# Kernel optimization log

Measured on AMD Instinct MI355X. Metric: run time of the kernel, lower is better.

Reference implementation:

```python
import jax, jax.numpy as jnp
import numpy as np

N_GROUP = 4
TOPK_GROUP = 2
TOP_K = 6
ROUTED_SCALE = 2.0

T, H, E, I = 1024, 1024, 16, 704
SHARED_I = 2 * H  # n_shared_experts * hidden_size


def setup_inputs() -> dict:
    key = jax.random.key(0)
    ks = jax.random.split(key, 10)
    s = 0.02
    return {
        "h": jax.random.normal(ks[0], (T, H), jnp.float32),
        "gate_w": jax.random.normal(ks[1], (E, H), jnp.float32) * s,
        "bias": jax.random.normal(ks[2], (E,), jnp.float32) * 0.1,
        "wg": jax.random.normal(ks[3], (E, H, I), jnp.float32) * s,
        "wu": jax.random.normal(ks[4], (E, H, I), jnp.float32) * s,
        "wd": jax.random.normal(ks[5], (E, I, H), jnp.float32) * s,
        "swg": jax.random.normal(ks[6], (H, SHARED_I), jnp.float32) * s,
        "swu": jax.random.normal(ks[7], (H, SHARED_I), jnp.float32) * s,
        "swd": jax.random.normal(ks[8], (SHARED_I, H), jnp.float32) * s,
    }


def _moe_forward(h, gate_w, bias, wg, wu, wd, swg, swu, swd):
    Tn, Hd = h.shape
    En = gate_w.shape[0]
    per_group = En // N_GROUP

    # shared expert (SwiGLU MLP)
    shared = (jax.nn.silu(h @ swg) * (h @ swu)) @ swd  # [T, H]

    # gate: noaux_tc biased grouped top-k routing (DeepSeek-V3 style)
    logits = h @ gate_w.T                      # [T, E]
    scores = jax.nn.sigmoid(logits)            # [T, E]
    scores_for_choice = scores + bias[None, :]
    grp = scores_for_choice.reshape(Tn, N_GROUP, per_group)
    group_scores = jnp.sum(jax.lax.top_k(grp, 2)[0], axis=-1)   # [T, G] top-2 sum
    _, top_groups = jax.lax.top_k(group_scores, TOPK_GROUP)     # [T, TG]
    gmask = jnp.zeros((Tn, N_GROUP), bool).at[
        jnp.arange(Tn)[:, None], top_groups].set(True)
    emask = jnp.repeat(gmask, per_group, axis=1)                # [T, E]
    masked = jnp.where(emask, scores_for_choice, -jnp.inf)
    _, topk_ids = jax.lax.top_k(masked, TOP_K)                  # [T, K]
    topk_w = jnp.take_along_axis(scores, topk_ids, axis=1)      # weights from unbiased scores
    topk_w = topk_w / jnp.sum(topk_w, axis=-1, keepdims=True)   # norm_topk_prob=True

    # sparse combine weights [T, E]
    cw = jnp.zeros((Tn, En), h.dtype).at[
        jnp.arange(Tn)[:, None], topk_ids].add(topk_w)

    # per-expert SwiGLU MLPs (dense over experts, sparse combine)
    g = jnp.einsum('th,ehi->tei', h, wg)
    u = jnp.einsum('th,ehi->tei', h, wu)
    y = jnp.einsum('tei,eih->teh', jax.nn.silu(g) * u, wd)
    routed = jnp.einsum('te,teh->th', cw, y)

    return routed * ROUTED_SCALE + shared


def reference(h, gate_w, bias, wg, wu, wd, swg, swu, swd):
    return _moe_forward(h, gate_w, bias, wg, wu, wd, swg, swu, swd)
```

## Files before the change

### kernel.cpp

```cpp
#include <hip/hip_runtime.h>
#include <hip/hip_bf16.h>
#include <math.h>

#define TT 1024
#define HH 1024
#define NEXP 16
#define NI 704
#define SI 2048
#define UPMAX 506
#define WDTILES 1408
#define DNSHARED 64
#define DNMAX (DNSHARED + 504)

typedef unsigned short us;
typedef __attribute__((ext_vector_type(8))) __bf16 bf16x8;
typedef __attribute__((ext_vector_type(8))) short s16x8;
typedef __attribute__((ext_vector_type(4))) float f32x4;
typedef __attribute__((ext_vector_type(4))) unsigned short us4;

__device__ __forceinline__ us f2bf(float f) {
  unsigned u = __builtin_bit_cast(unsigned, f);
  u += 0x7fffu + ((u >> 16) & 1u);
  return (us)(u >> 16);
}

__device__ __forceinline__ int ldsOff(int row, int kg) {
  return (row * 4 + (kg ^ ((row >> 1) & 3))) * 16;
}

__device__ __forceinline__ void gl16(const void* g, void* l) {
  __builtin_amdgcn_global_load_lds((const __attribute__((address_space(1))) void*)g,
                                   (__attribute__((address_space(3))) void*)l, 16, 0, 0);
}

__device__ __forceinline__ int chunkMap(int b, int n) {
  int q = n >> 3, r = n & 7;
  int c = b & 7, i = b >> 3;
  int base = (c < r) ? c * (q + 1) : r * (q + 1) + (c - r) * q;
  return base + i;
}

__device__ __forceinline__ void tconv_tile(const float* __restrict__ inz,
                                           us* __restrict__ outz,
                                           int C, int ldo, int r0, int c0,
                                           float (*tile)[65]) {
  int t = threadIdx.x;
  int rr = t >> 4, cc = (t & 15) * 4;
  #pragma unroll
  for (int i = 0; i < 4; ++i) {
    f32x4 v = *reinterpret_cast<const f32x4*>(inz + (size_t)(r0 + rr + i * 16) * C + c0 + cc);
    tile[rr + i*16][cc + 0] = v[0];
    tile[rr + i*16][cc + 1] = v[1];
    tile[rr + i*16][cc + 2] = v[2];
    tile[rr + i*16][cc + 3] = v[3];
  }
  __syncthreads();
  int c = t >> 2, rq = t & 3;
  us lo[8], hi[8];
  #pragma unroll
  for (int j = 0; j < 8; ++j) {
    lo[j] = f2bf(tile[rq * 8 + j][c]);
    hi[j] = f2bf(tile[32 + rq * 8 + j][c]);
  }
  us* op = outz + (size_t)(c0 + c) * ldo + r0;
  *reinterpret_cast<s16x8*>(op + rq * 8)      = *reinterpret_cast<s16x8*>(&lo[0]);
  *reinterpret_cast<s16x8*>(op + 32 + rq * 8) = *reinterpret_cast<s16x8*>(&hi[0]);
}

__device__ __forceinline__ void tconv512(const float* __restrict__ inz,
                                         us* __restrict__ outz,
                                         int i0, int h0, float (*tile)[129]) {
  int t = threadIdx.x;
  int ir = t >> 3, cg = (t & 7) * 4;
  #pragma unroll
  for (int p = 0; p < 4; ++p) {
    f32x4 v = *reinterpret_cast<const f32x4*>(inz + (size_t)(i0 + ir) * HH + h0 + cg + p * 32);
    tile[ir][cg + p*32 + 0] = v[0];
    tile[ir][cg + p*32 + 1] = v[1];
    tile[ir][cg + p*32 + 2] = v[2];
    tile[ir][cg + p*32 + 3] = v[3];
  }
  __syncthreads();
  int c = t >> 2, rq = t & 3;
  us lo[8], hi[8];
  #pragma unroll
  for (int j = 0; j < 8; ++j) {
    lo[j] = f2bf(tile[rq * 8 + j][c]);
    hi[j] = f2bf(tile[32 + rq * 8 + j][c]);
  }
  us* op = outz + (size_t)(h0 + c) * NI + i0;
  *reinterpret_cast<s16x8*>(op + rq * 8)      = *reinterpret_cast<s16x8*>(&lo[0]);
  *reinterpret_cast<s16x8*>(op + 32 + rq * 8) = *reinterpret_cast<s16x8*>(&hi[0]);
}

__global__ __launch_bounds__(256) void k_prep(
    const float* __restrict__ h, const float* __restrict__ gw,
    const float* __restrict__ bias, float* __restrict__ cw,
    us* __restrict__ hb, unsigned* __restrict__ selpk,
    const float* __restrict__ wg, const float* __restrict__ wu,
    const float* __restrict__ swg, const float* __restrict__ swu,
    us* __restrict__ wgb, us* __restrict__ wub,
    us* __restrict__ swgb, us* __restrict__ swub) {
  __shared__ float tile[64][65];
  __shared__ float lgS[NEXP];
  int b = blockIdx.x;
  int tid = threadIdx.x;
  if (b < 1024) {
    int t = b;
    const float* hr = h + (size_t)t * HH;
    {
      f32x4 v = *reinterpret_cast<const f32x4*>(hr + tid * 4);
      us4 p;
      p[0] = f2bf(v[0]); p[1] = f2bf(v[1]); p[2] = f2bf(v[2]); p[3] = f2bf(v[3]);
      *reinterpret_cast<us4*>(hb + (size_t)t * HH + tid * 4) = p;
    }
    int e = tid >> 4, sub = tid & 15;
    const f32x4* hr4 = reinterpret_cast<const f32x4*>(hr);
    const f32x4* gr4 = reinterpret_cast<const f32x4*>(gw + (size_t)e * HH);
    float acc = 0.f;
    for (int i = sub; i < 256; i += 16) {
      f32x4 a = hr4[i], g = gr4[i];
      acc += a[0]*g[0] + a[1]*g[1] + a[2]*g[2] + a[3]*g[3];
    }
    acc += __shfl_down(acc, 8, 16);
    acc += __shfl_down(acc, 4, 16);
    acc += __shfl_down(acc, 2, 16);
    acc += __shfl_down(acc, 1, 16);
    if (sub == 0) lgS[e] = acc;
    __syncthreads();
    if (tid == 0) {
      float sc[NEXP], s4[NEXP];
      for (int i = 0; i < NEXP; ++i) {
        sc[i] = 1.f / (1.f + expf(-lgS[i]));
        s4[i] = sc[i] + bias[i];
      }
      float gs[4];
      for (int g = 0; g < 4; ++g) {
        float a = s4[4*g], bb = s4[4*g+1], c = s4[4*g+2], d = s4[4*g+3];
        float mx01 = fmaxf(a, bb), mn01 = fminf(a, bb);
        float mx23 = fmaxf(c, d), mn23 = fminf(c, d);
        float top = fmaxf(mx01, mx23);
        float sec = (mx01 >= mx23) ? fmaxf(mn01, mx23) : fmaxf(mn23, mx01);
        gs[g] = top + sec;
      }
      int g1 = 0;
      for (int g = 1; g < 4; ++g) if (gs[g] > gs[g1]) g1 = g;
      int g2 = -1;
      for (int g = 0; g < 4; ++g) { if (g == g1) continue; if (g2 < 0 || gs[g] > gs[g2]) g2 = g; }
      int sel[6];
      bool used[NEXP];
      for (int i = 0; i < NEXP; ++i) used[i] = false;
      float wsum = 0.f;
      for (int it = 0; it < 6; ++it) {
        int best = -1; float bv = 0.f;
        for (int i = 0; i < NEXP; ++i) {
          int grp = i >> 2;
          if ((grp != g1 && grp != g2) || used[i]) continue;
          if (best < 0 || s4[i] > bv) { best = i; bv = s4[i]; }
        }
        used[best] = true;
        sel[it] = best;
        wsum += sc[best];
      }
      float inv = 2.0f / wsum;
      unsigned pk = 0;
      for (int it = 0; it < 6; ++it) {
        pk |= (unsigned)sel[it] << (it * 4);
        cw[(size_t)t * NEXP + sel[it]] = sc[sel[it]] * inv;
      }
      selpk[t] = pk;
    }
    return;
  }
  b -= 1024;
  if (b < 2816) {
    int z = b / 176, r = b % 176;
    tconv_tile(wg + (size_t)z * HH * NI, wgb + (size_t)z * NI * HH,
               NI, HH, (r / 11) * 64, (r % 11) * 64, tile);
    return;
  }
  b -= 2816;
  if (b < 2816) {
    int z = b / 176, r = b % 176;
    tconv_tile(wu + (size_t)z * HH * NI, wub + (size_t)z * NI * HH,
               NI, HH, (r / 11) * 64, (r % 11) * 64, tile);
    return;
  }
  b -= 2816;
  if (b < 512) {
    tconv_tile(swg, swgb, SI, HH, (b >> 5) * 64, (b & 31) * 64, tile);
    return;
  }
  b -= 512;
  {
    tconv_tile(swu, swub, SI, HH, (b >> 5) * 64, (b & 31) * 64, tile);
  }
}

__global__ void k_scan(const unsigned* __restrict__ selpk,
                       int* __restrict__ cnt, int* __restrict__ list,
                       int* __restrict__ wlUp, int* __restrict__ wlDn,
                       int* __restrict__ totals) {
  int t = threadIdx.x;
  int w = t >> 6, l = t & 63;
  unsigned pk = selpk[t];
  unsigned short flags = 0;
  #pragma unroll
  for (int j = 0; j < 6; ++j) flags |= (unsigned short)(1u << ((pk >> (j * 4)) & 15));
  __shared__ int wc[16][16];
  __shared__ int pre[16][16];
  __shared__ int tiles_s[16], upo[16], dno[16], totR[2];
  #pragma unroll
  for (int e = 0; e < 16; ++e) {
    unsigned long long bal = __ballot((flags >> e) & 1);
    if (l == 0) wc[w][e] = __popcll(bal);
  }
  __syncthreads();
  if (t < 16) {
    int s = 0;
    for (int ww = 0; ww < 16; ++ww) { pre[ww][t] = s; s += wc[ww][t]; }
    cnt[t] = s;
    tiles_s[t] = (s + 127) >> 7;
  }
  __syncthreads();
  if (t < 16) {
    int uo = 0, dn = 0;
    for (int e2 = 0; e2 < t; ++e2) { uo += 6 * tiles_s[e2]; dn += 8 * tiles_s[e2]; }
    upo[t] = uo; dno[t] = dn;
    if (t == 15) { totR[0] = uo + 6 * tiles_s[15]; totR[1] = dn + 8 * tiles_s[15]; }
  }
  __syncthreads();
  {
    int te = tiles_s[w];
    for (int i = l; i < 6 * te; i += 64) {
      int nt = i / te, mt = i - nt * te;
      wlUp[upo[w] + i] = ((w * 6 + nt) << 3) | mt;
    }
    for (int i = l; i < 8 * te; i += 64) {
      int nt = i / te, mt = i - nt * te;
      wlDn[dno[w] + i] = ((w * 8 + nt) << 3) | mt;
    }
  }
  if (w == 0) {
    for (int j = l; j < 128; j += 64)
      wlUp[totR[0] + j] = ((96 + (j >> 3)) << 3) | (j & 7);
  }
  if (t == 0) { totals[0] = totR[0] + 128; totals[1] = totR[1]; }
  unsigned long long lmask = (l == 0) ? 0ull : ((~0ull) >> (64 - l));
  #pragma unroll
  for (int e = 0; e < 16; ++e) {
    bool f = (flags >> e) & 1;
    unsigned long long bal = __ballot(f);
    if (f) {
      int rank = __popcll(bal & lmask);
      int j = 0;
      #pragma unroll
      for (int jj = 0; jj < 6; ++jj) j += (((pk >> (jj * 4)) & 15) == (unsigned)e) ? jj : 0;
      list[(e << 10) + pre[w][e] + rank] = (t << 3) | j;
    }
  }
}

__global__ void k_tconvS(const float* __restrict__ swd, us* __restrict__ swdT) {
  __shared__ float tile[64][65];
  int b = blockIdx.x;
  tconv_tile(swd, swdT, HH, SI, (b >> 4) * 64, (b & 15) * 64, tile);
}

__global__ __launch_bounds__(512) void k_upT(
    const us* __restrict__ hb,
    const us* __restrict__ wgb, const us* __restrict__ wub,
    const us* __restrict__ swgb, const us* __restrict__ swub,
    const float* __restrict__ cw, const int* __restrict__ list,
    const int* __restrict__ cnt, const int* __restrict__ wlUp,
    const int* __restrict__ totals,
    us* __restrict__ cact_r, us* __restrict__ cact_s,
    const float* __restrict__ wd, us* __restrict__ wdbT) {
  __shared__ __align__(16) char ldsb[73728];
  int tid = threadIdx.x;
  if ((int)blockIdx.x >= UPMAX) {
    int b = blockIdx.x - UPMAX;
    int z = b / 88, r = b % 88;
    tconv512(wd + (size_t)z * NI * HH, wdbT + (size_t)z * HH * NI,
             (r >> 3) * 64, (r & 7) * 128,
             reinterpret_cast<float(*)[129]>(ldsb));
    return;
  }
  int tot = totals[0];
  if ((int)blockIdx.x >= tot) return;
  int item = wlUp[chunkMap(blockIdx.x, tot)];
  int group = item >> 3, mt = item & 7;
  int t0 = mt * 128;
  bool routed = group < 96;
  int e = 0, n0, cntE = TT;
  const us *bgBase, *buBase;
  if (routed) {
    e = group / 6;
    n0 = (group - e * 6) * 128;
    cntE = cnt[e];
    bgBase = wgb + (size_t)e * NI * HH;
    buBase = wub + (size_t)e * NI * HH;
  } else {
    n0 = (group - 96) * 128;
    bgBase = swgb;
    buBase = swub;
  }
  int w = tid >> 6, l = tid & 63;
  int wm = w >> 2, wn = w & 3;
  int lr = l & 15, lg2 = l >> 4;

  int rowA = tid >> 2;
  int kg = (tid & 3) ^ ((rowA >> 1) & 3);
  int tok = t0 + rowA;
  if (routed) tok = (tok < cntE) ? (list[(e << 10) + tok] >> 3) : 0;
  int bRow = n0 + rowA;
  if (routed && bRow >= NI) bRow = NI - 1;
  const us* aS = hb + (size_t)tok * HH + kg * 8;
  const us* gS = bgBase + (size_t)bRow * HH + kg * 8;
  const us* uS = buBase + (size_t)bRow * HH + kg * 8;

  f32x4 accG[4][2] = {};
  f32x4 accU[4][2] = {};

  int wslot = w * 1024;
  auto stage = [&](char* buf) {
    char* b = buf + wslot;
    gl16(aS, b);
    gl16(gS, b + 8192);
    gl16(uS, b + 16384);
    aS += 32; gS += 32; uS += 32;
  };

  char* bA = ldsb;
  char* bB = ldsb + 24576;
  char* bC = ldsb + 49152;
  stage(bA);
  stage(bB);
  for (int ki = 0; ki < 32; ++ki) {
    if (ki < 30) {
      stage(bC);
      asm volatile("s_waitcnt vmcnt(6)" ::: "memory");
    } else if (ki == 30) {
      asm volatile("s_waitcnt vmcnt(3)" ::: "memory");
    } else {
      asm volatile("s_waitcnt vmcnt(0)" ::: "memory");
    }
    __builtin_amdgcn_s_barrier();
    asm volatile("" ::: "memory");
    bf16x8 af[4], bg[2], bu[2];
    #pragma unroll
    for (int rf = 0; rf < 4; ++rf)
      af[rf] = *reinterpret_cast<const bf16x8*>(bA + ldsOff(wm * 64 + rf * 16 + lr, lg2));
    #pragma unroll
    for (int cf = 0; cf < 2; ++cf) {
      int n = wn * 32 + cf * 16 + lr;
      bg[cf] = *reinterpret_cast<const bf16x8*>(bA + 8192  + ldsOff(n, lg2));
      bu[cf] = *reinterpret_cast<const bf16x8*>(bA + 16384 + ldsOff(n, lg2));
    }
    __builtin_amdgcn_s_setprio(1);
    #pragma unroll
    for (int rf = 0; rf < 4; ++rf)
      #pragma unroll
      for (int cf = 0; cf < 2; ++cf) {
        accG[rf][cf] = __builtin_amdgcn_mfma_f32_16x16x32_bf16(af[rf], bg[cf], accG[rf][cf], 0, 0, 0);
        accU[rf][cf] = __builtin_amdgcn_mfma_f32_16x16x32_bf16(af[rf], bu[cf], accU[rf][cf], 0, 0, 0);
      }
    __builtin_amdgcn_s_setprio(0);
    __builtin_amdgcn_s_barrier();
    asm volatile("" ::: "memory");
    char* tp = bA; bA = bB; bB = bC; bC = tp;
  }
  #pragma unroll
  for (int rf = 0; rf < 4; ++rf)
    #pragma unroll
    for (int cf = 0; cf < 2; ++cf)
      #pragma unroll
      for (int r = 0; r < 4; ++r) {
        int row = wm * 64 + rf * 16 + lg2 * 4 + r;
        int col = wn * 32 + cf * 16 + lr;
        float g = accG[rf][cf][r], u = accU[rf][cf][r];
        float act = g / (1.f + __expf(-g)) * u;
        if (routed) {
          int slot = t0 + row;
          if (slot < cntE && n0 + col < NI) {
            int packed = list[(e << 10) + slot];
            float scl = cw[(size_t)(packed >> 3) * NEXP + e];
            cact_r[((size_t)(e << 10) + slot) * NI + n0 + col] = f2bf(act * scl);
          }
        } else {
          cact_s[(size_t)(t0 + row) * SI + n0 + col] = f2bf(act);
        }
      }
}

__global__ __launch_bounds__(256) void k_down(
    const us* __restrict__ cact_r, const us* __restrict__ cact_s,
    const us* __restrict__ wdbT, const us* __restrict__ swdT,
    const int* __restrict__ list, const int* __restrict__ cnt,
    const int* __restrict__ wlDn, const int* __restrict__ totals,
    us* __restrict__ part, float* __restrict__ out) {
  __shared__ __align__(16) char ldsb[49152];
  int tid = threadIdx.x;
  int b = blockIdx.x;
  bool routed;
  int e = 0, nt, mt, kiter, Ksrc, cntE = TT;
  const us *Ab, *Bb;
  if (b < DNSHARED) {
    routed = false;
    nt = b & 7;
    mt = b >> 3;
    kiter = 64;
    Ksrc = SI;
    Ab = cact_s;
    Bb = swdT;
  } else {
    routed = true;
    int rb = b - DNSHARED;
    int tot = totals[1];
    if (rb >= tot) return;
    int item = wlDn[chunkMap(rb, tot)];
    int group = item >> 3;
    mt = item & 7;
    e = group >> 3; nt = group & 7;
    cntE = cnt[e];
    kiter = NI / 32;
    Ksrc = NI;
    Ab = cact_r + (size_t)e * 1024 * NI;
    Bb = wdbT + (size_t)e * 1024 * NI;
  }
  int t0 = mt * 128;
  int n0 = nt * 128;
  int w = tid >> 6, l = tid & 63;
  int wm = w >> 1, wn = w & 1;
  int lr = l & 15, lg2 = l >> 4;

  int rowA = tid >> 2;
  int kg = (tid & 3) ^ ((rowA >> 1) & 3);
  const us* aS0 = Ab + (size_t)(t0 + rowA) * Ksrc + kg * 8;
  const us* aS1 = Ab + (size_t)(t0 + 64 + rowA) * Ksrc + kg * 8;
  const us* bS0 = Bb + (size_t)(n0 + rowA) * Ksrc + kg * 8;
  const us* bS1 = Bb + (size_t)(n0 + 64 + rowA) * Ksrc + kg * 8;

  f32x4 acc[4][4] = {};

  int wslot = w * 1024;
  auto stage = [&](char* buf) {
    char* bp = buf + wslot;
    gl16(aS0, bp);
    gl16(aS1, bp + 4096);
    gl16(bS0, bp + 8192);
    gl16(bS1, bp + 12288);
    aS0 += 32; aS1 += 32; bS0 += 32; bS1 += 32;
  };

  char* bA = ldsb;
  char* bB = ldsb + 16384;
  char* bC = ldsb + 32768;
  stage(bA);
  stage(bB);
  for (int ki = 0; ki < kiter; ++ki) {
    if (ki + 2 < kiter) {
      stage(bC);
      asm volatile("s_waitcnt vmcnt(8)" ::: "memory");
    } else if (ki + 2 == kiter) {
      asm volatile("s_waitcnt vmcnt(4)" ::: "memory");
    } else {
      asm volatile("s_waitcnt vmcnt(0)" ::: "memory");
    }
    __builtin_amdgcn_s_barrier();
    asm volatile("" ::: "memory");
    bf16x8 af[4], bb[4];
    #pragma unroll
    for (int rf = 0; rf < 4; ++rf)
      af[rf] = *reinterpret_cast<const bf16x8*>(bA + ldsOff(wm * 64 + rf * 16 + lr, lg2));
    #pragma unroll
    for (int cf = 0; cf < 4; ++cf)
      bb[cf] = *reinterpret_cast<const bf16x8*>(bA + 8192 + ldsOff(wn * 64 + cf * 16 + lr, lg2));
    __builtin_amdgcn_s_setprio(1);
    #pragma unroll
    for (int rf = 0; rf < 4; ++rf)
      #pragma unroll
      for (int cf = 0; cf < 4; ++cf)
        acc[rf][cf] = __builtin_amdgcn_mfma_f32_16x16x32_bf16(af[rf], bb[cf], acc[rf][cf], 0, 0, 0);
    __builtin_amdgcn_s_setprio(0);
    __builtin_amdgcn_s_barrier();
    asm volatile("" ::: "memory");
    char* tp = bA; bA = bB; bB = bC; bC = tp;
  }
  #pragma unroll
  for (int rf = 0; rf < 4; ++rf)
    #pragma unroll
    for (int cf = 0; cf < 4; ++cf)
      #pragma unroll
      for (int r = 0; r < 4; ++r) {
        int row = wm * 64 + rf * 16 + lg2 * 4 + r;
        int col = wn * 64 + cf * 16 + lr;
        if (routed) {
          int slot = t0 + row;
          if (slot < cntE) {
            int packed = list[(e << 10) + slot];
            int t = packed >> 3, j = packed & 7;
            part[((size_t)t * 6 + j) * 1024 + n0 + col] = f2bf(acc[rf][cf][r]);
          }
        } else {
          out[(size_t)(t0 + row) * HH + n0 + col] = acc[rf][cf][r];
        }
      }
}

__global__ void k_reduce(const us* __restrict__ part, float* __restrict__ out) {
  int i = (blockIdx.x * blockDim.x + threadIdx.x) * 4;
  int t = i >> 10, hh = i & 1023;
  f32x4 s = *reinterpret_cast<const f32x4*>(out + i);
  #pragma unroll
  for (int j = 0; j < 6; ++j) {
    us4 p = *reinterpret_cast<const us4*>(part + ((size_t)t * 6 + j) * 1024 + hh);
    #pragma unroll
    for (int k = 0; k < 4; ++k)
      s[k] += __builtin_bit_cast(float, (unsigned)p[k] << 16);
  }
  *reinterpret_cast<f32x4*>(out + i) = s;
}

#define HB_OFF    0ULL
#define CW_OFF    2097152ULL
#define CNT_OFF   2162688ULL
#define SELPK_OFF 2166784ULL
#define LIST_OFF  2170880ULL
#define WLUP_OFF  2236416ULL
#define WLDN_OFF  2244608ULL
#define TOT_OFF   2252800ULL
#define CACTR_OFF 2260992ULL
#define CACTS_OFF 25329664ULL
#define WGB_OFF   29523968ULL
#define WUB_OFF   52592640ULL
#define SWGB_OFF  75661312ULL
#define SWUB_OFF  79855616ULL
#define WDBT_OFF  84049920ULL
#define SWDT_OFF  SWGB_OFF
#define PART_OFF  WGB_OFF

extern "C" void kernel_launch(void* const* d_in, const int* in_sizes, int n_in,
                              void* d_out, int out_size, void* d_ws, size_t ws_size,
                              hipStream_t stream) {
  const float* h    = (const float*)d_in[0];
  const float* gw   = (const float*)d_in[1];
  const float* bias = (const float*)d_in[2];
  const float* wg   = (const float*)d_in[3];
  const float* wu   = (const float*)d_in[4];
  const float* wd   = (const float*)d_in[5];
  const float* swg  = (const float*)d_in[6];
  const float* swu  = (const float*)d_in[7];
  const float* swd  = (const float*)d_in[8];
  float* out = (float*)d_out;

  char* ws = (char*)d_ws;
  us*       hb     = (us*)(ws + HB_OFF);
  float*    cw     = (float*)(ws + CW_OFF);
  int*      cnt    = (int*)(ws + CNT_OFF);
  unsigned* selpk  = (unsigned*)(ws + SELPK_OFF);
  int*      list   = (int*)(ws + LIST_OFF);
  int*      wlUp   = (int*)(ws + WLUP_OFF);
  int*      wlDn   = (int*)(ws + WLDN_OFF);
  int*      totals = (int*)(ws + TOT_OFF);
  us*       cact_r = (us*)(ws + CACTR_OFF);
  us*       cact_s = (us*)(ws + CACTS_OFF);
  us*       wgb    = (us*)(ws + WGB_OFF);
  us*       wub    = (us*)(ws + WUB_OFF);
  us*       swgb   = (us*)(ws + SWGB_OFF);
  us*       swub   = (us*)(ws + SWUB_OFF);
  us*       wdbT   = (us*)(ws + WDBT_OFF);
  us*       swdT   = (us*)(ws + SWDT_OFF);
  us*       part   = (us*)(ws + PART_OFF);

  k_prep<<<7680, 256, 0, stream>>>(h, gw, bias, cw, hb, selpk,
                                   wg, wu, swg, swu, wgb, wub, swgb, swub);
  k_scan<<<1, 1024, 0, stream>>>(selpk, cnt, list, wlUp, wlDn, totals);

  k_upT<<<UPMAX + WDTILES, 512, 0, stream>>>(hb, wgb, wub, swgb, swub, cw, list,
                                             cnt, wlUp, totals, cact_r, cact_s,
                                             wd, wdbT);

  k_tconvS<<<512, 256, 0, stream>>>(swd, swdT);

  k_down<<<DNMAX, 256, 0, stream>>>(cact_r, cact_s, wdbT, swdT, list, cnt,
                                    wlDn, totals, part, out);
  k_reduce<<<1024, 256, 0, stream>>>(part, out);
}
```

Baseline: 130.4 us.

## Fuse fp32-to-bf16 weight conversion into up-projection GEMM operand loads

Removes the separate transpose/convert pass for gate/up weights (routed and shared) from the prep kernel. The up GEMM now reads fp32 weights directly from global memory into registers, converts them with packed bf16 conversion instructions, and writes them into LDS, double-buffering only the activation tile. This drops a full read-write pass over the gate/up weights and halves LDS use. In exchange it uses strided scalar fp32 loads, a shallower pipeline and extra VALU work inside the GEMM loop. Weights are re-read and re-converted once per token tile.

```diff
diff --git a/kernel.cpp b/kernel.cpp
--- a/kernel.cpp
+++ b/kernel.cpp
@@ -17,11 +17,18 @@
 typedef __attribute__((ext_vector_type(8))) short s16x8;
 typedef __attribute__((ext_vector_type(4))) float f32x4;
 typedef __attribute__((ext_vector_type(4))) unsigned short us4;
+typedef __attribute__((ext_vector_type(4))) unsigned int u32x4;
 
 __device__ __forceinline__ us f2bf(float f) {
   unsigned u = __builtin_bit_cast(unsigned, f);
   u += 0x7fffu + ((u >> 16) & 1u);
   return (us)(u >> 16);
+}
+
+__device__ __forceinline__ unsigned cvtpk(float lo, float hi) {
+  unsigned r;
+  asm volatile("v_cvt_pk_bf16_f32 %0, %1, %2" : "=v"(r) : "v"(lo), "v"(hi));
+  return r;
 }
 
 __device__ __forceinline__ int ldsOff(int row, int kg) {
@@ -93,107 +100,75 @@
   *reinterpret_cast<s16x8*>(op + 32 + rq * 8) = *reinterpret_cast<s16x8*>(&hi[0]);
 }
 
-__global__ __launch_bounds__(256) void k_prep(
+__global__ __launch_bounds__(256) void k_gate(
     const float* __restrict__ h, const float* __restrict__ gw,
     const float* __restrict__ bias, float* __restrict__ cw,
-    us* __restrict__ hb, unsigned* __restrict__ selpk,
-    const float* __restrict__ wg, const float* __restrict__ wu,
-    const float* __restrict__ swg, const float* __restrict__ swu,
-    us* __restrict__ wgb, us* __restrict__ wub,
-    us* __restrict__ swgb, us* __restrict__ swub) {
-  __shared__ float tile[64][65];
+    us* __restrict__ hb, unsigned* __restrict__ selpk) {
   __shared__ float lgS[NEXP];
-  int b = blockIdx.x;
+  int t = blockIdx.x;
   int tid = threadIdx.x;
-  if (b < 1024) {
-    int t = b;
-    const float* hr = h + (size_t)t * HH;
-    {
-      f32x4 v = *reinterpret_cast<const f32x4*>(hr + tid * 4);
-      us4 p;
-      p[0] = f2bf(v[0]); p[1] = f2bf(v[1]); p[2] = f2bf(v[2]); p[3] = f2bf(v[3]);
-      *reinterpret_cast<us4*>(hb + (size_t)t * HH + tid * 4) = p;
-    }
-    int e = tid >> 4, sub = tid & 15;
-    const f32x4* hr4 = reinterpret_cast<const f32x4*>(hr);
-    const f32x4* gr4 = reinterpret_cast<const f32x4*>(gw + (size_t)e * HH);
-    float acc = 0.f;
-    for (int i = sub; i < 256; i += 16) {
-      f32x4 a = hr4[i], g = gr4[i];
-      acc += a[0]*g[0] + a[1]*g[1] + a[2]*g[2] + a[3]*g[3];
-    }
-    acc += __shfl_down(acc, 8, 16);
-    acc += __shfl_down(acc, 4, 16);
-    acc += __shfl_down(acc, 2, 16);
-    acc += __shfl_down(acc, 1, 16);
-    if (sub == 0) lgS[e] = acc;
-    __syncthreads();
-    if (tid == 0) {
-      float sc[NEXP], s4[NEXP];
+  const float* hr = h + (size_t)t * HH;
+  {
+    f32x4 v = *reinterpret_cast<const f32x4*>(hr + tid * 4);
+    us4 p;
+    p[0] = f2bf(v[0]); p[1] = f2bf(v[1]); p[2] = f2bf(v[2]); p[3] = f2bf(v[3]);
+    *reinterpret_cast<us4*>(hb + (size_t)t * HH + tid * 4) = p;
+  }
+  int e = tid >> 4, sub = tid & 15;
+  const f32x4* hr4 = reinterpret_cast<const f32x4*>(hr);
+  const f32x4* gr4 = reinterpret_cast<const f32x4*>(gw + (size_t)e * HH);
+  float acc = 0.f;
+  for (int i = sub; i < 256; i += 16) {
+    f32x4 a = hr4[i], g = gr4[i];
+    acc += a[0]*g[0] + a[1]*g[1] + a[2]*g[2] + a[3]*g[3];
+  }
+  acc += __shfl_down(acc, 8, 16);
+  acc += __shfl_down(acc, 4, 16);
+  acc += __shfl_down(acc, 2, 16);
+  acc += __shfl_down(acc, 1, 16);
+  if (sub == 0) lgS[e] = acc;
+  __syncthreads();
+  if (tid == 0) {
+    float sc[NEXP], s4[NEXP];
+    for (int i = 0; i < NEXP; ++i) {
+      sc[i] = 1.f / (1.f + expf(-lgS[i]));
+      s4[i] = sc[i] + bias[i];
+    }
+    float gs[4];
+    for (int g = 0; g < 4; ++g) {
+      float a = s4[4*g], bb = s4[4*g+1], c = s4[4*g+2], d = s4[4*g+3];
+      float mx01 = fmaxf(a, bb), mn01 = fminf(a, bb);
+      float mx23 = fmaxf(c, d), mn23 = fminf(c, d);
+      float top = fmaxf(mx01, mx23);
+      float sec = (mx01 >= mx23) ? fmaxf(mn01, mx23) : fmaxf(mn23, mx01);
+      gs[g] = top + sec;
+    }
+    int g1 = 0;
+    for (int g = 1; g < 4; ++g) if (gs[g] > gs[g1]) g1 = g;
+    int g2 = -1;
+    for (int g = 0; g < 4; ++g) { if (g == g1) continue; if (g2 < 0 || gs[g] > gs[g2]) g2 = g; }
+    int sel[6];
+    bool used[NEXP];
+    for (int i = 0; i < NEXP; ++i) used[i] = false;
+    float wsum = 0.f;
+    for (int it = 0; it < 6; ++it) {
+      int best = -1; float bv = 0.f;
       for (int i = 0; i < NEXP; ++i) {
-        sc[i] = 1.f / (1.f + expf(-lgS[i]));
-        s4[i] = sc[i] + bias[i];
+        int grp = i >> 2;
+        if ((grp != g1 && grp != g2) || used[i]) continue;
+        if (best < 0 || s4[i] > bv) { best = i; bv = s4[i]; }
       }
-      float gs[4];
-      for (int g = 0; g < 4; ++g) {
-        float a = s4[4*g], bb = s4[4*g+1], c = s4[4*g+2], d = s4[4*g+3];
-        float mx01 = fmaxf(a, bb), mn01 = fminf(a, bb);
-        float mx23 = fmaxf(c, d), mn23 = fminf(c, d);
-        float top = fmaxf(mx01, mx23);
-        float sec = (mx01 >= mx23) ? fmaxf(mn01, mx23) : fmaxf(mn23, mx01);
-        gs[g] = top + sec;
-      }
-      int g1 = 0;
-      for (int g = 1; g < 4; ++g) if (gs[g] > gs[g1]) g1 = g;
-      int g2 = -1;
-      for (int g = 0; g < 4; ++g) { if (g == g1) continue; if (g2 < 0 || gs[g] > gs[g2]) g2 = g; }
-      int sel[6];
-      bool used[NEXP];
-      for (int i = 0; i < NEXP; ++i) used[i] = false;
-      float wsum = 0.f;
-      for (int it = 0; it < 6; ++it) {
-        int best = -1; float bv = 0.f;
-        for (int i = 0; i < NEXP; ++i) {
-          int grp = i >> 2;
-          if ((grp != g1 && grp != g2) || used[i]) continue;
-          if (best < 0 || s4[i] > bv) { best = i; bv = s4[i]; }
-        }
-        used[best] = true;
-        sel[it] = best;
-        wsum += sc[best];
-      }
-      float inv = 2.0f / wsum;
-      unsigned pk = 0;
-      for (int it = 0; it < 6; ++it) {
-        pk |= (unsigned)sel[it] << (it * 4);
-        cw[(size_t)t * NEXP + sel[it]] = sc[sel[it]] * inv;
-      }
-      selpk[t] = pk;
-    }
-    return;
-  }
-  b -= 1024;
-  if (b < 2816) {
-    int z = b / 176, r = b % 176;
-    tconv_tile(wg + (size_t)z * HH * NI, wgb + (size_t)z * NI * HH,
-               NI, HH, (r / 11) * 64, (r % 11) * 64, tile);
-    return;
-  }
-  b -= 2816;
-  if (b < 2816) {
-    int z = b / 176, r = b % 176;
-    tconv_tile(wu + (size_t)z * HH * NI, wub + (size_t)z * NI * HH,
-               NI, HH, (r / 11) * 64, (r % 11) * 64, tile);
-    return;
-  }
-  b -= 2816;
-  if (b < 512) {
-    tconv_tile(swg, swgb, SI, HH, (b >> 5) * 64, (b & 31) * 64, tile);
-    return;
-  }
-  b -= 512;
-  {
-    tconv_tile(swu, swub, SI, HH, (b >> 5) * 64, (b & 31) * 64, tile);
+      used[best] = true;
+      sel[it] = best;
+      wsum += sc[best];
+    }
+    float inv = 2.0f / wsum;
+    unsigned pk = 0;
+    for (int it = 0; it < 6; ++it) {
+      pk |= (unsigned)sel[it] << (it * 4);
+      cw[(size_t)t * NEXP + sel[it]] = sc[sel[it]] * inv;
+    }
+    selpk[t] = pk;
   }
 }
 
@@ -269,14 +244,14 @@
 
 __global__ __launch_bounds__(512) void k_upT(
     const us* __restrict__ hb,
-    const us* __restrict__ wgb, const us* __restrict__ wub,
-    const us* __restrict__ swgb, const us* __restrict__ swub,
+    const float* __restrict__ wg, const float* __restrict__ wu,
+    const float* __restrict__ swg, const float* __restrict__ swu,
     const float* __restrict__ cw, const int* __restrict__ list,
     const int* __restrict__ cnt, const int* __restrict__ wlUp,
     const int* __restrict__ totals,
     us* __restrict__ cact_r, us* __restrict__ cact_s,
     const float* __restrict__ wd, us* __restrict__ wdbT) {
-  __shared__ __align__(16) char ldsb[73728];
+  __shared__ __align__(16) char ldsb[36864];
   int tid = threadIdx.x;
   if ((int)blockIdx.x >= UPMAX) {
     int b = blockIdx.x - UPMAX;
@@ -292,83 +267,109 @@
   int group = item >> 3, mt = item & 7;
   int t0 = mt * 128;
   bool routed = group < 96;
-  int e = 0, n0, cntE = TT;
-  const us *bgBase, *buBase;
+  int e = 0, n0, cntE = TT, ldB;
+  const float *BgF, *BuF;
   if (routed) {
     e = group / 6;
     n0 = (group - e * 6) * 128;
     cntE = cnt[e];
-    bgBase = wgb + (size_t)e * NI * HH;
-    buBase = wub + (size_t)e * NI * HH;
+    ldB = NI;
+    BgF = wg + (size_t)e * HH * NI;
+    BuF = wu + (size_t)e * HH * NI;
   } else {
     n0 = (group - 96) * 128;
-    bgBase = swgb;
-    buBase = swub;
+    ldB = SI;
+    BgF = swg;
+    BuF = swu;
   }
   int w = tid >> 6, l = tid & 63;
   int wm = w >> 2, wn = w & 3;
   int lr = l & 15, lg2 = l >> 4;
 
   int rowA = tid >> 2;
-  int kg = (tid & 3) ^ ((rowA >> 1) & 3);
+  int kgA = (tid & 3) ^ ((rowA >> 1) & 3);
   int tok = t0 + rowA;
   if (routed) tok = (tok < cntE) ? (list[(e << 10) + tok] >> 3) : 0;
-  int bRow = n0 + rowA;
-  if (routed && bRow >= NI) bRow = NI - 1;
-  const us* aS = hb + (size_t)tok * HH + kg * 8;
-  const us* gS = bgBase + (size_t)bRow * HH + kg * 8;
-  const us* uS = buBase + (size_t)bRow * HH + kg * 8;
+  const us* aS = hb + (size_t)tok * HH + kgA * 8;
+
+  int nB = tid & 127;
+  int kgB = tid >> 7;
+  int nn = n0 + nB;
+  if (routed && nn >= NI) nn = NI - 1;
+  const float* gSrc = BgF + (size_t)kgB * 8 * ldB + nn;
+  const float* uSrc = BuF + (size_t)kgB * 8 * ldB + nn;
+  int bOff = ldsOff(nB, kgB);
+
+  char* bufA0 = ldsb;
+  char* bufA1 = ldsb + 8192;
+  char* bufBg = ldsb + 16384;
+  char* bufBu = ldsb + 24576;
+  int wslot = w * 1024;
 
   f32x4 accG[4][2] = {};
   f32x4 accU[4][2] = {};
 
-  int wslot = w * 1024;
-  auto stage = [&](char* buf) {
-    char* b = buf + wslot;
-    gl16(aS, b);
-    gl16(gS, b + 8192);
-    gl16(uS, b + 16384);
-    aS += 32; gS += 32; uS += 32;
-  };
-
-  char* bA = ldsb;
-  char* bB = ldsb + 24576;
-  char* bC = ldsb + 49152;
-  stage(bA);
-  stage(bB);
+  float bg[8], bu[8];
+  #pragma unroll
+  for (int j = 0; j < 8; ++j) bg[j] = gSrc[(size_t)j * ldB];
+  #pragma unroll
+  for (int j = 0; j < 8; ++j) bu[j] = uSrc[(size_t)j * ldB];
+  gSrc += 32 * (size_t)ldB; uSrc += 32 * (size_t)ldB;
+  gl16(aS, bufA0 + wslot);
+  aS += 32;
+
+  char* bufAr = bufA0;
+  char* bufAw = bufA1;
   for (int ki = 0; ki < 32; ++ki) {
-    if (ki < 30) {
-      stage(bC);
-      asm volatile("s_waitcnt vmcnt(6)" ::: "memory");
-    } else if (ki == 30) {
-      asm volatile("s_waitcnt vmcnt(3)" ::: "memory");
+    {
+      unsigned pg[4], pu[4];
+      #pragma unroll
+      for (int q = 0; q < 4; ++q) {
+        pg[q] = cvtpk(bg[2*q], bg[2*q+1]);
+        pu[q] = cvtpk(bu[2*q], bu[2*q+1]);
+      }
+      u32x4 vg = {pg[0], pg[1], pg[2], pg[3]};
+      u32x4 vu = {pu[0], pu[1], pu[2], pu[3]};
+      *reinterpret_cast<u32x4*>(bufBg + bOff) = vg;
+      *reinterpret_cast<u32x4*>(bufBu + bOff) = vu;
+    }
+    if (ki < 31) {
+      #pragma unroll
+      for (int j = 0; j < 8; ++j) bg[j] = gSrc[(size_t)j * ldB];
+      #pragma unroll
+      for (int j = 0; j < 8; ++j) bu[j] = uSrc[(size_t)j * ldB];
+      gSrc += 32 * (size_t)ldB; uSrc += 32 * (size_t)ldB;
+      gl16(aS, bufAw + wslot);
+      aS += 32;
+      asm volatile("s_waitcnt vmcnt(17)" ::: "memory");
     } else {
       asm volatile("s_waitcnt vmcnt(0)" ::: "memory");
     }
+    asm volatile("s_waitcnt lgkmcnt(0)" ::: "memory");
     __builtin_amdgcn_s_barrier();
     asm volatile("" ::: "memory");
-    bf16x8 af[4], bg[2], bu[2];
+    bf16x8 af[4], bgf[2], buf[2];
     #pragma unroll
     for (int rf = 0; rf < 4; ++rf)
-      af[rf] = *reinterpret_cast<const bf16x8*>(bA + ldsOff(wm * 64 + rf * 16 + lr, lg2));
+      af[rf] = *reinterpret_cast<const bf16x8*>(bufAr + ldsOff(wm * 64 + rf * 16 + lr, lg2));
     #pragma unroll
     for (int cf = 0; cf < 2; ++cf) {
       int n = wn * 32 + cf * 16 + lr;
-      bg[cf] = *reinterpret_cast<const bf16x8*>(bA + 8192  + ldsOff(n, lg2));
-      bu[cf] = *reinterpret_cast<const bf16x8*>(bA + 16384 + ldsOff(n, lg2));
+      bgf[cf] = *reinterpret_cast<const bf16x8*>(bufBg + ldsOff(n, lg2));
+      buf[cf] = *reinterpret_cast<const bf16x8*>(bufBu + ldsOff(n, lg2));
     }
     __builtin_amdgcn_s_setprio(1);
     #pragma unroll
     for (int rf = 0; rf < 4; ++rf)
       #pragma unroll
       for (int cf = 0; cf < 2; ++cf) {
-        accG[rf][cf] = __builtin_amdgcn_mfma_f32_16x16x32_bf16(af[rf], bg[cf], accG[rf][cf], 0, 0, 0);
-        accU[rf][cf] = __builtin_amdgcn_mfma_f32_16x16x32_bf16(af[rf], bu[cf], accU[rf][cf], 0, 0, 0);
+        accG[rf][cf] = __builtin_amdgcn_mfma_f32_16x16x32_bf16(af[rf], bgf[cf], accG[rf][cf], 0, 0, 0);
+        accU[rf][cf] = __builtin_amdgcn_mfma_f32_16x16x32_bf16(af[rf], buf[cf], accU[rf][cf], 0, 0, 0);
       }
     __builtin_amdgcn_s_setprio(0);
     __builtin_amdgcn_s_barrier();
     asm volatile("" ::: "memory");
-    char* tp = bA; bA = bB; bB = bC; bC = tp;
+    char* tp = bufAr; bufAr = bufAw; bufAw = tp;
   }
   #pragma unroll
   for (int rf = 0; rf < 4; ++rf)
@@ -533,9 +534,7 @@
 #define CACTR_OFF 2260992ULL
 #define CACTS_OFF 25329664ULL
 #define WGB_OFF   29523968ULL
-#define WUB_OFF   52592640ULL
 #define SWGB_OFF  75661312ULL
-#define SWUB_OFF  79855616ULL
 #define WDBT_OFF  84049920ULL
 #define SWDT_OFF  SWGB_OFF
 #define PART_OFF  WGB_OFF
@@ -565,19 +564,14 @@
   int*      totals = (int*)(ws + TOT_OFF);
   us*       cact_r = (us*)(ws + CACTR_OFF);
   us*       cact_s = (us*)(ws + CACTS_OFF);
-  us*       wgb    = (us*)(ws + WGB_OFF);
-  us*       wub    = (us*)(ws + WUB_OFF);
-  us*       swgb   = (us*)(ws + SWGB_OFF);
-  us*       swub   = (us*)(ws + SWUB_OFF);
   us*       wdbT   = (us*)(ws + WDBT_OFF);
   us*       swdT   = (us*)(ws + SWDT_OFF);
   us*       part   = (us*)(ws + PART_OFF);
 
-  k_prep<<<7680, 256, 0, stream>>>(h, gw, bias, cw, hb, selpk,
-                                   wg, wu, swg, swu, wgb, wub, swgb, swub);
+  k_gate<<<1024, 256, 0, stream>>>(h, gw, bias, cw, hb, selpk);
   k_scan<<<1, 1024, 0, stream>>>(selpk, cnt, list, wlUp, wlDn, totals);
 
-  k_upT<<<UPMAX + WDTILES, 512, 0, stream>>>(hb, wgb, wub, swgb, swub, cw, list,
+  k_upT<<<UPMAX + WDTILES, 512, 0, stream>>>(hb, wg, wu, swg, swu, cw, list,
                                              cnt, wlUp, totals, cact_r, cact_s,
                                              wd, wdbT);
 
```

After: 130.5 us. About the same (+0.1%).
